# Kernel optimization log

Hardware: AMD Instinct MI355X
Metric: run time of the kernel (lower is better)

The kernel has to match this reference:

```python
import jax, jax.numpy as jnp
import numpy as np

B, L, D = 16, 2048, 128
GROUP = 16
NG = L // GROUP  # number of groups per batch
ALPHA = 0.5


def setup_inputs() -> dict:
    key = jax.random.key(0)
    k0, k1, k2 = jax.random.split(key, 3)
    x = jax.random.normal(k0, (B, L, D), dtype=jnp.float32)
    # per-batch permutation = gather indices (each position used exactly once)
    group_tensor = jax.vmap(lambda k: jax.random.permutation(k, L))(
        jax.random.split(k1, B)).astype(jnp.int32)
    ctxlens = jnp.full((B,), L, dtype=jnp.int32)
    W = jax.random.normal(k2, (2 * D,), dtype=jnp.float32) * (1.0 / np.sqrt(D))
    norm_alpha = jnp.ones((2,), dtype=jnp.float32)
    norm_gamma = jnp.ones((2 * D,), dtype=jnp.float32)
    norm_beta = jnp.zeros((2 * D,), dtype=jnp.float32)
    return {"x": x, "group_tensor": group_tensor, "ctxlens": ctxlens, "W": W,
            "norm_alpha": norm_alpha, "norm_gamma": norm_gamma, "norm_beta": norm_beta}


def _leaky_relu(v):
    return jnp.where(v >= 0, v, 0.01 * v)


def _ncn_forward(x, group_tensor, ctxlens, W, norm_alpha, norm_gamma, norm_beta):
    Bd, Ld, Dd = x.shape
    ng = Ld // GROUP
    Wi, Wj = W[:Dd], W[Dd:]
    a1, a2 = norm_alpha[0], norm_alpha[1]
    g1, g2 = norm_gamma[:Dd], norm_gamma[Dd:]
    b1, b2 = norm_beta[:Dd], norm_beta[Dd:]

    # gather x by group indices -> [B, NG, GROUP, D]
    xg = jnp.take_along_axis(x, group_tensor[:, :, None].astype(jnp.int32), axis=1)
    xg = xg.reshape(Bd, ng, GROUP, Dd)

    def step(carry, j):
        xi, xa = carry  # each [B, NG, GROUP, D]
        xj = jax.lax.dynamic_slice_in_dim(xi, j, 1, axis=2)  # [B, NG, 1, D]
        sim = jnp.einsum('bgnd,d->bgn', xi, Wi) \
            + jnp.einsum('bgd,d->bg', xj[:, :, 0, :], Wj)[:, :, None]  # [B,NG,GROUP]
        T = ALPHA * xi + (1.0 - ALPHA) * sim[..., None] * xj
        T_norm = g1 * jnp.tanh(a1 * T) + b1
        Fv = _leaky_relu(T_norm)
        xa = xa + Fv                               # ya = xa + F
        xi = xi + g2 * jnp.tanh(a2 * xa) + b2      # yi = xi + norm2(ya)
        return (xi, xa), None

    (yi, ya), _ = jax.lax.scan(step, (xg, jnp.zeros_like(xg)), jnp.arange(GROUP))

    # kernel only processes/stores a group if its start offset < ctxlen
    valid = (jnp.arange(ng, dtype=jnp.int32) * GROUP)[None, :] < ctxlens[:, None]
    yi = jnp.where(valid[:, :, None, None], yi, 0.0).reshape(Bd, Ld, Dd)
    ya = jnp.where(valid[:, :, None, None], ya, 0.0).reshape(Bd, Ld, Dd)

    # scatter back to original positions
    bidx = jnp.arange(Bd)[:, None]
    yi_out = jnp.zeros_like(x).at[bidx, group_tensor].set(yi)
    ya_out = jnp.zeros_like(x).at[bidx, group_tensor].set(ya)
    return yi_out, ya_out


def reference(x, group_tensor, ctxlens, W, norm_alpha, norm_gamma, norm_beta):
    return _ncn_forward(x, group_tensor, ctxlens, W, norm_alpha, norm_gamma, norm_beta)
```

## Files before the change

### kernel.cpp

```cpp
#include <hip/hip_runtime.h>

#define B_ 16
#define L_ 2048
#define D_ 128
#define GROUP_ 16
#define NG_ (L_ / GROUP_)
#define LOG2E_ 1.44269504088896340736f

template<int CTRL>
__device__ __forceinline__ float dpp_add(float v) {
    int x = __builtin_amdgcn_update_dpp(0, __float_as_int(v), CTRL, 0xF, 0xF, false);
    return v + __int_as_float(x);
}
__device__ __forceinline__ float row16_sum(float v) {
    v = dpp_add<0xB1>(v);
    v = dpp_add<0x4E>(v);
    v = dpp_add<0x141>(v);
    v = dpp_add<0x140>(v);
    return v;
}

__device__ __forceinline__ void rcp8(const float d[8], float r[8]) {
    float p[8];
    p[0] = d[0];
#pragma unroll
    for (int k = 1; k < 8; ++k) p[k] = p[k - 1] * d[k];
    float R = __builtin_amdgcn_rcpf(p[7]);
#pragma unroll
    for (int k = 7; k >= 1; --k) { r[k] = p[k - 1] * R; R *= d[k]; }
    r[0] = R;
}

__global__ __launch_bounds__(256, 4) void ncn_kernel(
    const float* __restrict__ x,
    const int*   __restrict__ gt,
    const int*   __restrict__ ctxlens,
    const float* __restrict__ W,
    const float* __restrict__ nalpha,
    const float* __restrict__ ngamma,
    const float* __restrict__ nbeta,
    float* __restrict__ out)
{
    const int blk = blockIdx.x;
    const int b   = blk >> 7;
    const int g   = blk & (NG_ - 1);
    const int tid = threadIdx.x;
    const int row = tid >> 4;
    const int rl  = tid & 15;
    const int d0  = rl << 3;

    __shared__ float s_xj[GROUP_][D_];
    __shared__ int   s_flag[GROUP_];

    if (tid < GROUP_) s_flag[tid] = 0;

    const float a1 = nalpha[0];
    const float a2 = nalpha[1];
    const float ca = -a1 * LOG2E_;
    const float S  = -2.0f * a2 * LOG2E_;
    const bool  selMin = (S < 0.0f);

    float Wi[8], Wj[8], G1S[8], B1S[8], G2[8], B2[8];
    {
        float g1r[8], b1r[8], g2r[8], b2r[8];
        *(float4*)&Wi[0]  = *(const float4*)(W + d0);
        *(float4*)&Wi[4]  = *(const float4*)(W + d0 + 4);
        *(float4*)&Wj[0]  = *(const float4*)(W + D_ + d0);
        *(float4*)&Wj[4]  = *(const float4*)(W + D_ + d0 + 4);
        *(float4*)&g1r[0] = *(const float4*)(ngamma + d0);
        *(float4*)&g1r[4] = *(const float4*)(ngamma + d0 + 4);
        *(float4*)&g2r[0] = *(const float4*)(ngamma + D_ + d0);
        *(float4*)&g2r[4] = *(const float4*)(ngamma + D_ + d0 + 4);
        *(float4*)&b1r[0] = *(const float4*)(nbeta + d0);
        *(float4*)&b1r[4] = *(const float4*)(nbeta + d0 + 4);
        *(float4*)&b2r[0] = *(const float4*)(nbeta + D_ + d0);
        *(float4*)&b2r[4] = *(const float4*)(nbeta + D_ + d0 + 4);
#pragma unroll
        for (int k = 0; k < 8; ++k) {
            G1S[k] = S * 2.0f * g1r[k];
            B1S[k] = S * (b1r[k] - g1r[k]);
            G2[k]  = 2.0f * g2r[k];
            B2[k]  = b2r[k] - g2r[k];
        }
    }

    const int l   = g * GROUP_ + row;
    const int tok = gt[b * L_ + l];
    const float* xp = x + ((size_t)(b * L_ + tok)) * D_ + d0;

    float xi[8], za[8];
    *(float4*)&xi[0] = *(const float4*)xp;
    *(float4*)&xi[4] = *(const float4*)(xp + 4);
#pragma unroll
    for (int k = 0; k < 8; ++k) za[k] = 0.0f;

    __syncthreads();

    volatile int* vflag = (volatile int*)s_flag;

    if (row == 0) {
        *(float4*)&s_xj[0][d0]     = *(float4*)&xi[0];
        *(float4*)&s_xj[0][d0 + 4] = *(float4*)&xi[4];
        __threadfence_block();
        if (rl == 0) vflag[0] = 1;
    }

    for (int j = 0; j < GROUP_; ++j) {
        while (vflag[j] == 0) { __builtin_amdgcn_s_sleep(1); }

        float xjv[8];
        *(float4*)&xjv[0] = *(const float4*)&s_xj[j][d0];
        *(float4*)&xjv[4] = *(const float4*)&s_xj[j][d0 + 4];

        float s = 0.0f;
#pragma unroll
        for (int k = 0; k < 8; ++k) s = fmaf(xi[k], Wi[k], s);
#pragma unroll
        for (int k = 0; k < 8; ++k) s = fmaf(xjv[k], Wj[k], s);
        s = row16_sum(s);
        const float cb = ca * s;

        float darr[8], r1[8];
#pragma unroll
        for (int k = 0; k < 8; ++k) {
            float u = fmaf(ca, xi[k], cb * xjv[k]);
            u = fminf(u, 15.0f);
            darr[k] = 1.0f + __builtin_amdgcn_exp2f(u);
        }
        rcp8(darr, r1);

#pragma unroll
        for (int k = 0; k < 8; ++k) {
            float tnS = fmaf(G1S[k], r1[k], B1S[k]);
            float alt = 0.01f * tnS;
            float FvS = selMin ? fminf(tnS, alt) : fmaxf(tnS, alt);
            za[k] += FvS;
            float z = fminf(za[k], 15.0f);
            darr[k] = 1.0f + __builtin_amdgcn_exp2f(z);
        }
        rcp8(darr, r1);

#pragma unroll
        for (int k = 0; k < 8; ++k)
            xi[k] += fmaf(G2[k], r1[k], B2[k]);

        if (row == j + 1) {
            *(float4*)&s_xj[j + 1][d0]     = *(float4*)&xi[0];
            *(float4*)&s_xj[j + 1][d0 + 4] = *(float4*)&xi[4];
            __threadfence_block();
            if (rl == 0) vflag[j + 1] = 1;
        }
    }

    const float invS = 1.0f / S;
    float xa[8];
#pragma unroll
    for (int k = 0; k < 8; ++k) xa[k] = za[k] * invS;

    const bool valid = (g * GROUP_) < ctxlens[b];
    if (!valid) {
#pragma unroll
        for (int k = 0; k < 8; ++k) { xi[k] = 0.0f; xa[k] = 0.0f; }
    }

    float* o1 = out + ((size_t)(b * L_ + tok)) * D_ + d0;
    float* o2 = o1 + (size_t)B_ * L_ * D_;
    *(float4*)o1       = *(float4*)&xi[0];
    *(float4*)(o1 + 4) = *(float4*)&xi[4];
    *(float4*)o2       = *(float4*)&xa[0];
    *(float4*)(o2 + 4) = *(float4*)&xa[4];
}

extern "C" void kernel_launch(void* const* d_in, const int* in_sizes, int n_in,
                              void* d_out, int out_size, void* d_ws, size_t ws_size,
                              hipStream_t stream) {
    const float* x  = (const float*)d_in[0];
    const int*   gt = (const int*)d_in[1];
    const int*   cl = (const int*)d_in[2];
    const float* W  = (const float*)d_in[3];
    const float* na = (const float*)d_in[4];
    const float* ng = (const float*)d_in[5];
    const float* nb = (const float*)d_in[6];
    float* out = (float*)d_out;

    ncn_kernel<<<B_ * NG_, 256, 0, stream>>>(x, gt, cl, W, na, ng, nb, out);
}
```

Before: 124.6 us.

## Interleave rows across waves and hoist xi-dependent dot off the critical path

```diff
diff --git a/kernel.cpp b/kernel.cpp
--- a/kernel.cpp
+++ b/kernel.cpp
@@ -45,7 +45,7 @@
     const int b   = blk >> 7;
     const int g   = blk & (NG_ - 1);
     const int tid = threadIdx.x;
-    const int row = tid >> 4;
+    const int row = (((tid >> 4) & 3) << 2) | (tid >> 6);
     const int rl  = tid & 15;
     const int d0  = rl << 3;
 
@@ -105,25 +105,39 @@
         if (rl == 0) vflag[0] = 1;
     }
 
+    float cx[8];
+    float sd;
+    {
+        float s = 0.0f, s2 = 0.0f;
+#pragma unroll
+        for (int k = 0; k < 4; ++k) s  = fmaf(xi[k], Wi[k], s);
+#pragma unroll
+        for (int k = 4; k < 8; ++k) s2 = fmaf(xi[k], Wi[k], s2);
+        sd = row16_sum(s + s2);
+#pragma unroll
+        for (int k = 0; k < 8; ++k) cx[k] = ca * xi[k];
+    }
+
     for (int j = 0; j < GROUP_; ++j) {
-        while (vflag[j] == 0) { __builtin_amdgcn_s_sleep(1); }
+        while (vflag[j] == 0) { }
+        __threadfence_block();
 
         float xjv[8];
         *(float4*)&xjv[0] = *(const float4*)&s_xj[j][d0];
         *(float4*)&xjv[4] = *(const float4*)&s_xj[j][d0 + 4];
 
-        float s = 0.0f;
-#pragma unroll
-        for (int k = 0; k < 8; ++k) s = fmaf(xi[k], Wi[k], s);
-#pragma unroll
-        for (int k = 0; k < 8; ++k) s = fmaf(xjv[k], Wj[k], s);
-        s = row16_sum(s);
-        const float cb = ca * s;
+        float s = 0.0f, s2 = 0.0f;
+#pragma unroll
+        for (int k = 0; k < 4; ++k) s  = fmaf(xjv[k], Wj[k], s);
+#pragma unroll
+        for (int k = 4; k < 8; ++k) s2 = fmaf(xjv[k], Wj[k], s2);
+        const float sim = sd + row16_sum(s + s2);
+        const float cb  = ca * sim;
 
         float darr[8], r1[8];
 #pragma unroll
         for (int k = 0; k < 8; ++k) {
-            float u = fmaf(ca, xi[k], cb * xjv[k]);
+            float u = fmaf(cb, xjv[k], cx[k]);
             u = fminf(u, 15.0f);
             darr[k] = 1.0f + __builtin_amdgcn_exp2f(u);
         }
@@ -144,12 +158,21 @@
         for (int k = 0; k < 8; ++k)
             xi[k] += fmaf(G2[k], r1[k], B2[k]);
 
-        if (row == j + 1) {
+        if (j < GROUP_ - 1 && row == j + 1) {
             *(float4*)&s_xj[j + 1][d0]     = *(float4*)&xi[0];
             *(float4*)&s_xj[j + 1][d0 + 4] = *(float4*)&xi[4];
             __threadfence_block();
             if (rl == 0) vflag[j + 1] = 1;
         }
+
+        float t = 0.0f, t2 = 0.0f;
+#pragma unroll
+        for (int k = 0; k < 4; ++k) t  = fmaf(xi[k], Wi[k], t);
+#pragma unroll
+        for (int k = 4; k < 8; ++k) t2 = fmaf(xi[k], Wi[k], t2);
+        sd = row16_sum(t + t2);
+#pragma unroll
+        for (int k = 0; k < 8; ++k) cx[k] = ca * xi[k];
     }
 
     const float invS = 1.0f / S;
```

Result: slower. 127.7 us (+2.5%).
